# Performance work log

Hardware: AMD Instinct MI355X
Metric: run time of the kernel (lower is better)

Reference implementation:

```python
import jax, jax.numpy as jnp
import numpy as np
import math

B, S, H, NH, HD = 2, 2048, 2048, 16, 128
ROPE_BASE = 10000.0

def _rope_cos_sin(seq_len, head_dim, base=ROPE_BASE, dtype=jnp.float32):
    inv_freq = 1.0 / (base ** (jnp.arange(0, head_dim, 2, dtype=jnp.float32) / head_dim))
    t = jnp.arange(seq_len, dtype=jnp.float32)
    freqs = jnp.outer(t, inv_freq)                      # [S, HD/2]
    emb = jnp.concatenate([freqs, freqs], axis=-1)      # [S, HD]
    return jnp.cos(emb).astype(dtype), jnp.sin(emb).astype(dtype)

def _rotate_half(x):
    d = x.shape[-1] // 2
    return jnp.concatenate([-x[..., d:], x[..., :d]], axis=-1)

def setup_inputs() -> dict:
    key = jax.random.key(0)
    ks = jax.random.split(key, 5)
    scale = 1.0 / math.sqrt(H)
    return {
        "input_tensor": jax.random.normal(ks[0], (B, S, H), dtype=jnp.float32),
        "attention_mask": jnp.ones((B, 1, S, S), dtype=jnp.float32),
        "Wq": jax.random.normal(ks[1], (H, H), dtype=jnp.float32) * scale,
        "Wk": jax.random.normal(ks[2], (H, H), dtype=jnp.float32) * scale,
        "Wv": jax.random.normal(ks[3], (H, H), dtype=jnp.float32) * scale,
        "Wo": jax.random.normal(ks[4], (H, H), dtype=jnp.float32) * scale,
    }

def reference(input_tensor, attention_mask, Wq, Wk, Wv, Wo):
    b, s, _ = input_tensor.shape
    scaling = 1.0 / math.sqrt(HD)
    # torch Linear: y = x @ W.T
    q = (input_tensor @ Wq.T).reshape(b, s, NH, HD).transpose(0, 2, 1, 3)  # [b,h,s,d]
    k = (input_tensor @ Wk.T).reshape(b, s, NH, HD).transpose(0, 2, 1, 3)
    v = (input_tensor @ Wv.T).reshape(b, s, NH, HD).transpose(0, 2, 1, 3)
    cos, sin = _rope_cos_sin(s, HD, dtype=input_tensor.dtype)  # [s,d]
    # faithful to source: RoPE is applied to query and VALUE states
    q = q * cos + _rotate_half(q) * sin
    v = v * cos + _rotate_half(v) * sin
    attn = jnp.einsum("bhqd,bhkd->bhqk", q, k) * scaling       # [b,h,s,s]
    attn = attn * attention_mask[:, :, :, :s]                  # multiplicative mask
    attn = jax.nn.softmax(attn.astype(jnp.float32), axis=-1).astype(q.dtype)
    out = jnp.einsum("bhqk,bhkd->bhqd", attn, v)               # [b,h,s,d]
    out = out.transpose(0, 2, 1, 3).reshape(b, s, NH * HD)
    return out @ Wo.T
```

## Files before the change

kernel.cpp:

```cpp
#include <hip/hip_runtime.h>


#define B_   2
#define S_   2048
#define H_   2048
#define NH_  16
#define HD_  128
#define BS_  4096
#define SCALE_ 0.08838834764831845f
#define SC2_   (SCALE_ * 1.4426950408889634f)
#define THR2_  11.0f

typedef unsigned short u16;
typedef unsigned int   u32;
typedef __attribute__((ext_vector_type(8))) short bf16x8;
typedef __attribute__((ext_vector_type(4))) float f32x4;

typedef __attribute__((address_space(1))) const u32 gu32;
typedef __attribute__((address_space(3))) u32 lu32;

__device__ __forceinline__ void gll16(const void* g, void* l) {
  __builtin_amdgcn_global_load_lds((gu32*)g, (lu32*)l, 16, 0, 0);
}

__device__ __forceinline__ u16 f2bf(float f) {
  union { float f; u32 u; } v; v.f = f;
  u32 r = v.u + 0x7fffu + ((v.u >> 16) & 1u);
  return (u16)(r >> 16);
}
__device__ __forceinline__ float bf2f(u16 u) {
  union { u32 u; float f; } v; v.u = ((u32)u) << 16;
  return v.f;
}

#if __has_builtin(__builtin_amdgcn_exp2f)
__device__ __forceinline__ float exp2_(float x) { return __builtin_amdgcn_exp2f(x); }
#else
__device__ __forceinline__ float exp2_(float x) { return exp2f(x); }
#endif

__global__ __launch_bounds__(256)
void k_prep(const float* __restrict__ X,  const float* __restrict__ Wq,
            const float* __restrict__ Wk, const float* __restrict__ Wv,
            u16* __restrict__ Xb,  u16* __restrict__ Wqb, u16* __restrict__ Wkb,
            u16* __restrict__ Wvb,
            float* __restrict__ cosT, float* __restrict__ sinT)
{
  const int y = blockIdx.y;
  if (y == 4) {
    const int i = blockIdx.x * 256 + threadIdx.x;
    if (i < S_ * 64) {
      const int s = i >> 6, d = i & 63;
      const float ang = (float)s * powf(10000.0f, -(float)d * (1.0f / 64.0f));
      cosT[i] = cosf(ang);
      sinT[i] = sinf(ang);
    }
    return;
  }
  const float* src; u16* dst; int n;
  if      (y == 0) { src = X;  dst = Xb;  n = 8388608; }
  else if (y == 1) { src = Wq; dst = Wqb; n = 4194304; }
  else if (y == 2) { src = Wk; dst = Wkb; n = 4194304; }
  else             { src = Wv; dst = Wvb; n = 4194304; }
  const int i = (blockIdx.x * 256 + threadIdx.x) * 4;
  if (i < n) {
    float4 v = *(const float4*)(src + i);
    u32 w0 = (u32)f2bf(v.x) | ((u32)f2bf(v.y) << 16);
    u32 w1 = (u32)f2bf(v.z) | ((u32)f2bf(v.w) << 16);
    *(uint2*)(dst + i) = make_uint2(w0, w1);
  }
}

__global__ __launch_bounds__(256)
void k_cvt(const float* __restrict__ in, u16* __restrict__ out, int n) {
  const int i = (blockIdx.x * 256 + threadIdx.x) * 4;
  if (i < n) {
    float4 v = *(const float4*)(in + i);
    u32 w0 = (u32)f2bf(v.x) | ((u32)f2bf(v.y) << 16);
    u32 w1 = (u32)f2bf(v.z) | ((u32)f2bf(v.w) << 16);
    *(uint2*)(out + i) = make_uint2(w0, w1);
  }
}

template<int QKV>
__global__ __launch_bounds__(256)
void k_gemm(const u16* __restrict__ A,
            const u16* __restrict__ W0, const u16* __restrict__ W1, const u16* __restrict__ W2,
            u16* __restrict__ oB0, u16* __restrict__ oB1, u16* __restrict__ oB2,
            float* __restrict__ oF)
{
  const u16* W;
  u16* outB = nullptr;
  if constexpr (QKV != 0) {
    const int z = blockIdx.z;
    W    = (z == 0) ? W0  : (z == 1) ? W1  : W2;
    outB = (z == 0) ? oB0 : (z == 1) ? oB1 : oB2;
  } else {
    W = W0;
  }
  constexpr int K = H_;
  constexpr int N = H_;

  __shared__ u16 lA[2][128 * 32];
  __shared__ u16 lB[2][128 * 32];
  const int tid  = threadIdx.x;
  const int lane = tid & 63;
  const int wr   = (tid >> 6) >> 1;
  const int wc   = (tid >> 6) & 1;
  const long m0 = (long)blockIdx.y * 128;
  const long n0 = (long)blockIdx.x * 128;
  constexpr int nkt = K >> 5;

  const int  eOff  = tid * 8;
  const int  srow  = eOff >> 5;
  const int  skc   = eOff & 31;
  const long aBase = (m0 + srow) * (long)K + skc;
  const long bBase = (n0 + srow) * (long)K + skc;

  f32x4 acc[4][4] = {};

#define STAGE_(kt_, buf_) do {                                   \
    long ko = (long)(kt_) * 32;                                  \
    gll16(A + aBase + ko,              &lA[buf_][eOff]);         \
    gll16(A + aBase + 64*(long)K + ko, &lA[buf_][2048 + eOff]);  \
    gll16(W + bBase + ko,              &lB[buf_][eOff]);         \
    gll16(W + bBase + 64*(long)K + ko, &lB[buf_][2048 + eOff]);  \
  } while (0)

  STAGE_(0, 0);
  __syncthreads();

  for (int kt = 0; kt < nkt; ++kt) {
    const int buf = kt & 1;
    if (kt + 1 < nkt) STAGE_(kt + 1, buf ^ 1);
    const int roff = lane & 15;
    const int koff = (lane >> 4) * 8;
    bf16x8 af[4], bfr[4];
#pragma unroll
    for (int m = 0; m < 4; ++m)
      af[m] = *(const bf16x8*)&lA[buf][(wr * 64 + m * 16 + roff) * 32 + koff];
#pragma unroll
    for (int n = 0; n < 4; ++n)
      bfr[n] = *(const bf16x8*)&lB[buf][(wc * 64 + n * 16 + roff) * 32 + koff];
#pragma unroll
    for (int m = 0; m < 4; ++m)
#pragma unroll
      for (int n = 0; n < 4; ++n)
        acc[m][n] = __builtin_amdgcn_mfma_f32_16x16x32_bf16(af[m], bfr[n], acc[m][n], 0, 0, 0);
    __syncthreads();
  }
#undef STAGE_

  const int cr = (lane >> 4) * 4;
  const int cc = lane & 15;
#pragma unroll
  for (int m = 0; m < 4; ++m) {
    const long row0 = m0 + wr * 64 + m * 16 + cr;
#pragma unroll
    for (int n = 0; n < 4; ++n) {
      const long col = n0 + wc * 64 + n * 16 + cc;
#pragma unroll
      for (int r = 0; r < 4; ++r) {
        if constexpr (QKV != 0) outB[(row0 + r) * N + col] = f2bf(acc[m][n][r]);
        else                    oF[(row0 + r) * N + col]   = acc[m][n][r];
      }
    }
  }
}

__global__ __launch_bounds__(256)
void k_rope_v_t(const u16* __restrict__ Vb, const float* __restrict__ cosT,
                const float* __restrict__ sinT, u16* __restrict__ Vt)
{
  __shared__ u16 tile[64][130];
  const int tid = threadIdx.x;
  const int kt = blockIdx.x, h = blockIdx.y, b = blockIdx.z;
#pragma unroll
  for (int p = 0; p < 4; ++p) {
    const int k  = p * 16 + (tid >> 4);
    const int d0 = (tid & 15) * 8;
    const long src = ((long)b * S_ + kt * 64 + k) * H_ + h * HD_ + d0;
    bf16x8 v = *(const bf16x8*)(Vb + src);
#pragma unroll
    for (int j = 0; j < 8; ++j) tile[k][d0 + j] = (u16)v[j];
  }
  __syncthreads();
  const long outByte = ((((long)b * NH_ + h) * 32 + kt) * 8192) * 2;
#pragma unroll
  for (int p = 0; p < 4; ++p) {
    const int idx = p * 256 + tid;
    const int d  = idx >> 3;
    const int k0 = (idx & 7) * 8;
    const int dm = d & 63;
    const float sgn = (d < 64) ? -1.0f : 1.0f;
    bf16x8 ov;
#pragma unroll
    for (int j = 0; j < 8; ++j) {
      const int k = k0 + j;
      const float c  = cosT[(kt * 64 + k) * 64 + dm];
      const float sn = sinT[(kt * 64 + k) * 64 + dm];
      const float x  = bf2f(tile[k][d]);
      const float xp = bf2f(tile[k][d ^ 64]);
      ov[j] = (short)f2bf(x * c + sgn * xp * sn);
    }
    const int m = d & 15;
    const int byteoff = (d >> 4) * 2048 + m * 128 + ((2 * k0) ^ ((m & 7) << 4));
    *(bf16x8*)((char*)Vt + outByte + byteoff) = ov;
  }
}

__global__ __launch_bounds__(256)
void k_flash(const u16* __restrict__ Qb, const u16* __restrict__ Kb,
             const u16* __restrict__ Vt, const float* __restrict__ mask,
             const float* __restrict__ cosT, const float* __restrict__ sinT,
             u16* __restrict__ AO)
{
  __shared__ u16 lK[64 * 128];
  __shared__ u16 lV[64 * 128];
  __shared__ u16 lP[4][16 * 64];
  const int tid = threadIdx.x, lane = tid & 63, wid = tid >> 6;
  const int qt = blockIdx.x, h = blockIdx.y, b = blockIdx.z;
  const long rowQ0 = (long)b * S_ + qt * 64 + wid * 16;
  const int qlr = (lane >> 4) * 4;

  bf16x8 qf[4];
  {
    const u16* qp = Qb + (rowQ0 + (lane & 15)) * H_ + h * HD_ + (lane >> 4) * 8;
#pragma unroll
    for (int s = 0; s < 4; ++s) qf[s] = *(const bf16x8*)(qp + s * 32);
    const int pos = qt * 64 + wid * 16 + (lane & 15);
    const float* cR = cosT + (pos << 6);
    const float* sR = sinT + (pos << 6);
#pragma unroll
    for (int s2 = 0; s2 < 2; ++s2) {
      const int dbase = s2 * 32 + (lane >> 4) * 8;
#pragma unroll
      for (int j = 0; j < 8; ++j) {
        const float c  = cR[dbase + j];
        const float sn = sR[dbase + j];
        const float x0 = bf2f((u16)qf[s2][j]);
        const float x1 = bf2f((u16)qf[s2 + 2][j]);
        qf[s2][j]     = (short)f2bf(x0 * c - x1 * sn);
        qf[s2 + 2][j] = (short)f2bf(x1 * c + x0 * sn);
      }
    }
  }

  f32x4 o[8] = {};
  float mrun[4], ssum[4];
#pragma unroll
  for (int r = 0; r < 4; ++r) { mrun[r] = -3.0e38f; ssum[r] = 0.0f; }

  const float* mrow[4];
#pragma unroll
  for (int r = 0; r < 4; ++r)
    mrow[r] = mask + (long)b * S_ * S_ + (long)(qt * 64 + wid * 16 + qlr + r) * S_;

  const long kgBase  = ((long)b * S_) * H_ + h * HD_;
  const long vtBase0 = (((long)b * NH_ + h) * 32) * 8192;
  const int  e0 = tid * 8;
  char* lKc = (char*)lK;
  char* lVc = (char*)lV;
  char* lPc = (char*)lP[wid];

  for (int kt = 0; kt < 32; ++kt) {
#pragma unroll
    for (int i = 0; i < 4; ++i) {
      int e   = i * 2048 + e0;
      int row = e >> 7;
      int gd  = (((e >> 3) & 15) ^ (row & 7)) << 3;
      gll16(Kb + kgBase + (long)(kt * 64 + row) * H_ + gd, (char*)lK + e * 2);
      gll16(Vt + vtBase0 + (long)kt * 8192 + e,            (char*)lV + e * 2);
    }
    __syncthreads();

    f32x4 sc[4] = {};
#pragma unroll
    for (int s = 0; s < 4; ++s) {
#pragma unroll
      for (int n = 0; n < 4; ++n) {
        const int row  = n * 16 + (lane & 15);
        const int byte = row * 256 + (((s * 64) + ((lane >> 4) * 16)) ^ ((row & 7) << 4));
        bf16x8 kf = *(const bf16x8*)(lKc + byte);
        sc[n] = __builtin_amdgcn_mfma_f32_16x16x32_bf16(qf[s], kf, sc[n], 0, 0, 0);
      }
    }

    const int kc0 = kt * 64;
    float y4[4][4];
#pragma unroll
    for (int r = 0; r < 4; ++r)
#pragma unroll
      for (int n = 0; n < 4; ++n)
        y4[n][r] = sc[n][r] * SC2_ * mrow[r][kc0 + n * 16 + (lane & 15)];

    float tmr[4];
#pragma unroll
    for (int r = 0; r < 4; ++r) {
      float tm = fmaxf(fmaxf(y4[0][r], y4[1][r]), fmaxf(y4[2][r], y4[3][r]));
      tm = fmaxf(tm, __shfl_xor(tm, 1, 64));
      tm = fmaxf(tm, __shfl_xor(tm, 2, 64));
      tm = fmaxf(tm, __shfl_xor(tm, 4, 64));
      tm = fmaxf(tm, __shfl_xor(tm, 8, 64));
      tmr[r] = tm;
    }
    const bool defer = (tmr[0] <= mrun[0] + THR2_) && (tmr[1] <= mrun[1] + THR2_) &&
                       (tmr[2] <= mrun[2] + THR2_) && (tmr[3] <= mrun[3] + THR2_);
    if (!__all(defer)) {
#pragma unroll
      for (int r = 0; r < 4; ++r) {
        const float mnew  = fmaxf(mrun[r], tmr[r]);
        const float alpha = exp2_(mrun[r] - mnew);
        mrun[r] = mnew;
        ssum[r] *= alpha;
#pragma unroll
        for (int df = 0; df < 8; ++df) o[df][r] *= alpha;
      }
    }
#pragma unroll
    for (int r = 0; r < 4; ++r) {
      float rs = 0.0f;
#pragma unroll
      for (int n = 0; n < 4; ++n) { float p = exp2_(y4[n][r] - mrun[r]); y4[n][r] = p; rs += p; }
      rs += __shfl_xor(rs, 1, 64);
      rs += __shfl_xor(rs, 2, 64);
      rs += __shfl_xor(rs, 4, 64);
      rs += __shfl_xor(rs, 8, 64);
      ssum[r] += rs;
    }

#pragma unroll
    for (int n = 0; n < 4; ++n) {
#pragma unroll
      for (int r = 0; r < 4; ++r) {
        const int q = qlr + r;
        const int byte = q * 128 + (((n * 16 + (lane & 15)) * 2) ^ ((q & 7) << 4));
        *(u16*)(lPc + byte) = f2bf(y4[n][r]);
      }
    }
    asm volatile("s_waitcnt lgkmcnt(0)" ::: "memory");
    __builtin_amdgcn_sched_barrier(0);

#pragma unroll
    for (int s2 = 0; s2 < 2; ++s2) {
      const int q  = lane & 15;
      const int pb = q * 128 + (((s2 * 64) + ((lane >> 4) * 16)) ^ ((q & 7) << 4));
      bf16x8 pf = *(const bf16x8*)(lPc + pb);
#pragma unroll
      for (int df = 0; df < 8; ++df) {
        const int m  = lane & 15;
        const int vb = df * 2048 + m * 128 + (((s2 * 64) + ((lane >> 4) * 16)) ^ ((m & 7) << 4));
        bf16x8 vf = *(const bf16x8*)(lVc + vb);
        o[df] = __builtin_amdgcn_mfma_f32_16x16x32_bf16(pf, vf, o[df], 0, 0, 0);
      }
    }
    __syncthreads();
  }

#pragma unroll
  for (int r = 0; r < 4; ++r) {
    const float inv = 1.0f / ssum[r];
    const long orow = (rowQ0 + qlr + r) * H_ + h * HD_;
#pragma unroll
    for (int df = 0; df < 8; ++df)
      AO[orow + df * 16 + (lane & 15)] = f2bf(o[df][r] * inv);
  }
}

extern "C" void kernel_launch(void* const* d_in, const int* in_sizes, int n_in,
                              void* d_out, int out_size, void* d_ws, size_t ws_size,
                              hipStream_t stream)
{
  const float* X    = (const float*)d_in[0];
  const float* mask = (const float*)d_in[1];
  const float* Wq   = (const float*)d_in[2];
  const float* Wk   = (const float*)d_in[3];
  const float* Wv   = (const float*)d_in[4];
  const float* Wo   = (const float*)d_in[5];
  float* out = (float*)d_out;
  char* ws = (char*)d_ws;

  u16* Xb    = (u16*)(ws + 0);
  u16* Wqb   = (u16*)(ws + 16777216);
  u16* Wkb   = (u16*)(ws + 25165824);
  u16* Wvb   = (u16*)(ws + 33554432);
  u16* Qb    = (u16*)(ws + 41943040);
  u16* Kb    = (u16*)(ws + 58720256);
  u16* Vb    = (u16*)(ws + 75497472);
  float* cosT = (float*)(ws + 92274688);
  float* sinT = (float*)(ws + 92798976);
  u16* Vt  = Wqb;
  u16* AO  = Xb;
  u16* Wob = Wvb;

  k_prep<<<dim3(8192, 5), 256, 0, stream>>>(X, Wq, Wk, Wv,
                                            Xb, Wqb, Wkb, Wvb, cosT, sinT);

  k_gemm<1><<<dim3(16, 32, 3), 256, 0, stream>>>(Xb, Wqb, Wkb, Wvb, Qb, Kb, Vb, nullptr);

  k_cvt<<<4096, 256, 0, stream>>>(Wo, Wob, 4194304);

  k_rope_v_t<<<dim3(32, 16, 2), 256, 0, stream>>>(Vb, cosT, sinT, Vt);

  k_flash<<<dim3(32, 16, 2), 256, 0, stream>>>(Qb, Kb, Vt, mask, cosT, sinT, AO);

  k_gemm<0><<<dim3(16, 32, 1), 256, 0, stream>>>(AO, Wob, nullptr, nullptr,
                                                 nullptr, nullptr, nullptr, out);
}
```

Baseline: 550.1 us.

## Double-buffer K/V tiles and process 32 query rows per wave in flash kernel

The flash-attention kernel now prefetches the next K/V tile into a second LDS buffer while computing the current one. It also doubles the query rows per wave (two 16-row subtiles) so each K/V fragment read from LDS feeds two MFMAs. The grid is halved to match. This trades more registers and LDS, and half as many blocks (512), for better latency hiding and more reuse of each K/V tile.

```diff
diff --git a/kernel.cpp b/kernel.cpp
--- a/kernel.cpp
+++ b/kernel.cpp
@@ -209,133 +209,155 @@
   }
 }
 
-__global__ __launch_bounds__(256)
+__global__ __launch_bounds__(256, 2)
 void k_flash(const u16* __restrict__ Qb, const u16* __restrict__ Kb,
              const u16* __restrict__ Vt, const float* __restrict__ mask,
              const float* __restrict__ cosT, const float* __restrict__ sinT,
              u16* __restrict__ AO)
 {
-  __shared__ u16 lK[64 * 128];
-  __shared__ u16 lV[64 * 128];
-  __shared__ u16 lP[4][16 * 64];
+  __shared__ u16 lK[2][64 * 128];
+  __shared__ u16 lV[2][64 * 128];
+  __shared__ u16 lP[4][32 * 64];
   const int tid = threadIdx.x, lane = tid & 63, wid = tid >> 6;
   const int qt = blockIdx.x, h = blockIdx.y, b = blockIdx.z;
-  const long rowQ0 = (long)b * S_ + qt * 64 + wid * 16;
-  const int qlr = (lane >> 4) * 4;
-
-  bf16x8 qf[4];
-  {
-    const u16* qp = Qb + (rowQ0 + (lane & 15)) * H_ + h * HD_ + (lane >> 4) * 8;
-#pragma unroll
-    for (int s = 0; s < 4; ++s) qf[s] = *(const bf16x8*)(qp + s * 32);
-    const int pos = qt * 64 + wid * 16 + (lane & 15);
+  const int l15 = lane & 15, hi = lane >> 4;
+  const long rowQ0 = (long)b * S_ + qt * 128 + wid * 32;
+  const int qlr = hi * 4;
+
+  bf16x8 qf[2][4];
+#pragma unroll
+  for (int sub = 0; sub < 2; ++sub) {
+    const u16* qp = Qb + (rowQ0 + sub * 16 + l15) * H_ + h * HD_ + hi * 8;
+#pragma unroll
+    for (int s = 0; s < 4; ++s) qf[sub][s] = *(const bf16x8*)(qp + s * 32);
+    const int pos = qt * 128 + wid * 32 + sub * 16 + l15;
     const float* cR = cosT + (pos << 6);
     const float* sR = sinT + (pos << 6);
 #pragma unroll
     for (int s2 = 0; s2 < 2; ++s2) {
-      const int dbase = s2 * 32 + (lane >> 4) * 8;
+      const int dbase = s2 * 32 + hi * 8;
 #pragma unroll
       for (int j = 0; j < 8; ++j) {
         const float c  = cR[dbase + j];
         const float sn = sR[dbase + j];
-        const float x0 = bf2f((u16)qf[s2][j]);
-        const float x1 = bf2f((u16)qf[s2 + 2][j]);
-        qf[s2][j]     = (short)f2bf(x0 * c - x1 * sn);
-        qf[s2 + 2][j] = (short)f2bf(x1 * c + x0 * sn);
-      }
-    }
-  }
-
-  f32x4 o[8] = {};
-  float mrun[4], ssum[4];
-#pragma unroll
-  for (int r = 0; r < 4; ++r) { mrun[r] = -3.0e38f; ssum[r] = 0.0f; }
-
-  const float* mrow[4];
-#pragma unroll
-  for (int r = 0; r < 4; ++r)
-    mrow[r] = mask + (long)b * S_ * S_ + (long)(qt * 64 + wid * 16 + qlr + r) * S_;
-
+        const float x0 = bf2f((u16)qf[sub][s2][j]);
+        const float x1 = bf2f((u16)qf[sub][s2 + 2][j]);
+        qf[sub][s2][j]     = (short)f2bf(x0 * c - x1 * sn);
+        qf[sub][s2 + 2][j] = (short)f2bf(x1 * c + x0 * sn);
+      }
+    }
+  }
+
+  f32x4 o[2][8] = {};
+  float mrun[2][4], ssum[2][4];
+#pragma unroll
+  for (int sub = 0; sub < 2; ++sub)
+#pragma unroll
+    for (int r = 0; r < 4; ++r) { mrun[sub][r] = -3.0e38f; ssum[sub][r] = 0.0f; }
+
+  const float* mbase = mask + (long)b * S_ * S_ + (long)(qt * 128 + wid * 32) * S_;
   const long kgBase  = ((long)b * S_) * H_ + h * HD_;
   const long vtBase0 = (((long)b * NH_ + h) * 32) * 8192;
   const int  e0 = tid * 8;
-  char* lKc = (char*)lK;
-  char* lVc = (char*)lV;
   char* lPc = (char*)lP[wid];
 
+#define FSTAGE_(kt_, bsel_) do {                                           \
+    _Pragma("unroll")                                                      \
+    for (int i_ = 0; i_ < 4; ++i_) {                                       \
+      int e_   = i_ * 2048 + e0;                                           \
+      int row_ = e_ >> 7;                                                  \
+      int gd_  = (((e_ >> 3) & 15) ^ (row_ & 7)) << 3;                     \
+      gll16(Kb + kgBase + (long)((kt_) * 64 + row_) * H_ + gd_,            \
+            (char*)lK[bsel_] + e_ * 2);                                    \
+      gll16(Vt + vtBase0 + (long)(kt_) * 8192 + e_,                        \
+            (char*)lV[bsel_] + e_ * 2);                                    \
+    }                                                                      \
+  } while (0)
+
+  FSTAGE_(0, 0);
+
   for (int kt = 0; kt < 32; ++kt) {
-#pragma unroll
-    for (int i = 0; i < 4; ++i) {
-      int e   = i * 2048 + e0;
-      int row = e >> 7;
-      int gd  = (((e >> 3) & 15) ^ (row & 7)) << 3;
-      gll16(Kb + kgBase + (long)(kt * 64 + row) * H_ + gd, (char*)lK + e * 2);
-      gll16(Vt + vtBase0 + (long)kt * 8192 + e,            (char*)lV + e * 2);
-    }
-    __syncthreads();
-
-    f32x4 sc[4] = {};
+    const int buf = kt & 1;
+    if (kt + 1 < 32) {
+      FSTAGE_(kt + 1, buf ^ 1);
+      asm volatile("s_waitcnt vmcnt(8)" ::: "memory");
+    } else {
+      asm volatile("s_waitcnt vmcnt(0)" ::: "memory");
+    }
+    __builtin_amdgcn_s_barrier();
+    __builtin_amdgcn_sched_barrier(0);
+    char* lKc = (char*)lK[buf];
+    char* lVc = (char*)lV[buf];
+
+    f32x4 sc[2][4] = {};
 #pragma unroll
     for (int s = 0; s < 4; ++s) {
 #pragma unroll
       for (int n = 0; n < 4; ++n) {
-        const int row  = n * 16 + (lane & 15);
-        const int byte = row * 256 + (((s * 64) + ((lane >> 4) * 16)) ^ ((row & 7) << 4));
+        const int row  = n * 16 + l15;
+        const int byte = row * 256 + (((s * 64) + hi * 16) ^ ((row & 7) << 4));
         bf16x8 kf = *(const bf16x8*)(lKc + byte);
-        sc[n] = __builtin_amdgcn_mfma_f32_16x16x32_bf16(qf[s], kf, sc[n], 0, 0, 0);
+        sc[0][n] = __builtin_amdgcn_mfma_f32_16x16x32_bf16(qf[0][s], kf, sc[0][n], 0, 0, 0);
+        sc[1][n] = __builtin_amdgcn_mfma_f32_16x16x32_bf16(qf[1][s], kf, sc[1][n], 0, 0, 0);
       }
     }
 
     const int kc0 = kt * 64;
-    float y4[4][4];
-#pragma unroll
-    for (int r = 0; r < 4; ++r)
-#pragma unroll
-      for (int n = 0; n < 4; ++n)
-        y4[n][r] = sc[n][r] * SC2_ * mrow[r][kc0 + n * 16 + (lane & 15)];
-
-    float tmr[4];
-#pragma unroll
-    for (int r = 0; r < 4; ++r) {
-      float tm = fmaxf(fmaxf(y4[0][r], y4[1][r]), fmaxf(y4[2][r], y4[3][r]));
-      tm = fmaxf(tm, __shfl_xor(tm, 1, 64));
-      tm = fmaxf(tm, __shfl_xor(tm, 2, 64));
-      tm = fmaxf(tm, __shfl_xor(tm, 4, 64));
-      tm = fmaxf(tm, __shfl_xor(tm, 8, 64));
-      tmr[r] = tm;
-    }
-    const bool defer = (tmr[0] <= mrun[0] + THR2_) && (tmr[1] <= mrun[1] + THR2_) &&
-                       (tmr[2] <= mrun[2] + THR2_) && (tmr[3] <= mrun[3] + THR2_);
-    if (!__all(defer)) {
+#pragma unroll
+    for (int sub = 0; sub < 2; ++sub) {
 #pragma unroll
       for (int r = 0; r < 4; ++r) {
-        const float mnew  = fmaxf(mrun[r], tmr[r]);
-        const float alpha = exp2_(mrun[r] - mnew);
-        mrun[r] = mnew;
-        ssum[r] *= alpha;
-#pragma unroll
-        for (int df = 0; df < 8; ++df) o[df][r] *= alpha;
-      }
-    }
-#pragma unroll
-    for (int r = 0; r < 4; ++r) {
-      float rs = 0.0f;
-#pragma unroll
-      for (int n = 0; n < 4; ++n) { float p = exp2_(y4[n][r] - mrun[r]); y4[n][r] = p; rs += p; }
-      rs += __shfl_xor(rs, 1, 64);
-      rs += __shfl_xor(rs, 2, 64);
-      rs += __shfl_xor(rs, 4, 64);
-      rs += __shfl_xor(rs, 8, 64);
-      ssum[r] += rs;
-    }
-
-#pragma unroll
-    for (int n = 0; n < 4; ++n) {
+        const float* mr = mbase + (long)(sub * 16 + qlr + r) * S_ + kc0;
+#pragma unroll
+        for (int n = 0; n < 4; ++n)
+          sc[sub][n][r] = sc[sub][n][r] * SC2_ * mr[n * 16 + l15];
+      }
+      float tmr[4];
 #pragma unroll
       for (int r = 0; r < 4; ++r) {
-        const int q = qlr + r;
-        const int byte = q * 128 + (((n * 16 + (lane & 15)) * 2) ^ ((q & 7) << 4));
-        *(u16*)(lPc + byte) = f2bf(y4[n][r]);
+        float tm = fmaxf(fmaxf(sc[sub][0][r], sc[sub][1][r]),
+                         fmaxf(sc[sub][2][r], sc[sub][3][r]));
+        tm = fmaxf(tm, __shfl_xor(tm, 1, 64));
+        tm = fmaxf(tm, __shfl_xor(tm, 2, 64));
+        tm = fmaxf(tm, __shfl_xor(tm, 4, 64));
+        tm = fmaxf(tm, __shfl_xor(tm, 8, 64));
+        tmr[r] = tm;
+      }
+      const bool defer = (tmr[0] <= mrun[sub][0] + THR2_) && (tmr[1] <= mrun[sub][1] + THR2_) &&
+                         (tmr[2] <= mrun[sub][2] + THR2_) && (tmr[3] <= mrun[sub][3] + THR2_);
+      if (!__all(defer)) {
+#pragma unroll
+        for (int r = 0; r < 4; ++r) {
+          const float mnew  = fmaxf(mrun[sub][r], tmr[r]);
+          const float alpha = exp2_(mrun[sub][r] - mnew);
+          mrun[sub][r] = mnew;
+          ssum[sub][r] *= alpha;
+#pragma unroll
+          for (int df = 0; df < 8; ++df) o[sub][df][r] *= alpha;
+        }
+      }
+#pragma unroll
+      for (int r = 0; r < 4; ++r) {
+        float rs = 0.0f;
+#pragma unroll
+        for (int n = 0; n < 4; ++n) {
+          float p = exp2_(sc[sub][n][r] - mrun[sub][r]);
+          sc[sub][n][r] = p; rs += p;
+        }
+        rs += __shfl_xor(rs, 1, 64);
+        rs += __shfl_xor(rs, 2, 64);
+        rs += __shfl_xor(rs, 4, 64);
+        rs += __shfl_xor(rs, 8, 64);
+        ssum[sub][r] += rs;
+      }
+#pragma unroll
+      for (int n = 0; n < 4; ++n) {
+#pragma unroll
+        for (int r = 0; r < 4; ++r) {
+          const int q = sub * 16 + qlr + r;
+          const int byte = q * 128 + (((n * 16 + l15) * 2) ^ ((q & 7) << 4));
+          *(u16*)(lPc + byte) = f2bf(sc[sub][n][r]);
+        }
       }
     }
     asm volatile("s_waitcnt lgkmcnt(0)" ::: "memory");
@@ -343,27 +365,36 @@
 
 #pragma unroll
     for (int s2 = 0; s2 < 2; ++s2) {
-      const int q  = lane & 15;
-      const int pb = q * 128 + (((s2 * 64) + ((lane >> 4) * 16)) ^ ((q & 7) << 4));
-      bf16x8 pf = *(const bf16x8*)(lPc + pb);
+      bf16x8 pf[2];
+#pragma unroll
+      for (int sub = 0; sub < 2; ++sub) {
+        const int q  = sub * 16 + l15;
+        const int pb = q * 128 + (((s2 * 64) + hi * 16) ^ ((q & 7) << 4));
+        pf[sub] = *(const bf16x8*)(lPc + pb);
+      }
 #pragma unroll
       for (int df = 0; df < 8; ++df) {
-        const int m  = lane & 15;
-        const int vb = df * 2048 + m * 128 + (((s2 * 64) + ((lane >> 4) * 16)) ^ ((m & 7) << 4));
+        const int vb = df * 2048 + l15 * 128 + (((s2 * 64) + hi * 16) ^ ((l15 & 7) << 4));
         bf16x8 vf = *(const bf16x8*)(lVc + vb);
-        o[df] = __builtin_amdgcn_mfma_f32_16x16x32_bf16(pf, vf, o[df], 0, 0, 0);
-      }
-    }
-    __syncthreads();
-  }
-
-#pragma unroll
-  for (int r = 0; r < 4; ++r) {
-    const float inv = 1.0f / ssum[r];
-    const long orow = (rowQ0 + qlr + r) * H_ + h * HD_;
-#pragma unroll
-    for (int df = 0; df < 8; ++df)
-      AO[orow + df * 16 + (lane & 15)] = f2bf(o[df][r] * inv);
+        o[0][df] = __builtin_amdgcn_mfma_f32_16x16x32_bf16(pf[0], vf, o[0][df], 0, 0, 0);
+        o[1][df] = __builtin_amdgcn_mfma_f32_16x16x32_bf16(pf[1], vf, o[1][df], 0, 0, 0);
+      }
+    }
+    asm volatile("s_waitcnt lgkmcnt(0)" ::: "memory");
+    __builtin_amdgcn_s_barrier();
+  }
+#undef FSTAGE_
+
+#pragma unroll
+  for (int sub = 0; sub < 2; ++sub) {
+#pragma unroll
+    for (int r = 0; r < 4; ++r) {
+      const float inv = 1.0f / ssum[sub][r];
+      const long orow = (rowQ0 + sub * 16 + qlr + r) * H_ + h * HD_;
+#pragma unroll
+      for (int df = 0; df < 8; ++df)
+        AO[orow + df * 16 + l15] = f2bf(o[sub][df][r] * inv);
+    }
   }
 }
 
@@ -402,7 +433,7 @@
 
   k_rope_v_t<<<dim3(32, 16, 2), 256, 0, stream>>>(Vb, cosT, sinT, Vt);
 
-  k_flash<<<dim3(32, 16, 2), 256, 0, stream>>>(Qb, Kb, Vt, mask, cosT, sinT, AO);
+  k_flash<<<dim3(16, 16, 2), 256, 0, stream>>>(Qb, Kb, Vt, mask, cosT, sinT, AO);
 
   k_gemm<0><<<dim3(16, 32, 1), 256, 0, stream>>>(AO, Wob, nullptr, nullptr,
                                                  nullptr, nullptr, nullptr, out);
```

New measurement: 629.6 us. 14.5% more time.
